# Kernel tuning notes

Measured on AMD Instinct MI355X. Metric: run time of the kernel, lower is better.

## Reference

```python
import jax, jax.numpy as jnp
import numpy as np

N_POINTS = 8192
N_DIM = 2
N_PAIRS = 262144


def setup_inputs() -> dict:
    key = jax.random.key(0)
    k1, k2, k3, k4 = jax.random.split(key, 4)
    logits = jax.random.normal(k1, (N_POINTS, N_DIM), dtype=jnp.float32)
    i = jax.random.randint(k2, (N_PAIRS,), 0, N_POINTS, dtype=jnp.int64)
    j = jax.random.randint(k3, (N_PAIRS,), 0, N_POINTS, dtype=jnp.int64)
    pij = jax.random.uniform(k4, (N_PAIRS,), dtype=jnp.float32, minval=1e-6, maxval=1.0)
    pij = pij / jnp.sum(pij)  # joint probabilities, strictly positive
    return {"pij": pij, "i": i, "j": j, "logits": logits}


def reference(pij, i, j, logits):
    # Pairwise squared distances via the norm expansion (same math as the
    # N x N x D expanded-subtract in the torch original, without the huge tensor).
    sq = jnp.sum(logits * logits, axis=1)                      # [N]
    dkl2 = sq[:, None] + sq[None, :] - 2.0 * (logits @ logits.T)  # [N, N]
    n_diag = logits.shape[0]
    # Student-t partition function, excluding the diagonal (each diag term is 1).
    part = jnp.sum(1.0 / (1.0 + dkl2)) - n_diag
    xi = logits[i]                                              # [E, D]
    xj = logits[j]                                              # [E, D]
    # NOTE: torch adds 1.0 elementwise BEFORE summing over D, so this is
    # (D + ||xi-xj||^2)^-1 — reproduced faithfully.
    num = 1.0 / jnp.sum(1.0 + (xi - xj) ** 2, axis=1)           # [E]
    qij = num / part
    return jnp.sum(pij * (jnp.log(pij) - jnp.log(qij)))
```

## Files before the change

kernel.cpp:

```cpp
#include <hip/hip_runtime.h>
#include <math.h>

#define N_POINTS 8192
#define N_PAIRS  262144

constexpr int BLOCKS  = 1024;
constexpr int THREADS = 256;
constexpr int TILE    = 4;
constexpr int NTILES  = N_POINTS / TILE;
constexpr int EPB     = N_PAIRS / BLOCKS;

typedef float f32x2 __attribute__((ext_vector_type(2)));

__global__ __launch_bounds__(THREADS)
void fused_kernel(const float* __restrict__ logits,
                  const float* __restrict__ pij,
                  const int* __restrict__ ei,
                  const int* __restrict__ ej,
                  float* __restrict__ partials) {
    __shared__ float wred[3][THREADS / 64];

    const int t = threadIdx.x;
    const int b = blockIdx.x;

    const int   ia = ei[b * EPB + t];
    const int   ja = ej[b * EPB + t];
    const float pp = pij[b * EPB + t];

    const float2* __restrict__ pts = (const float2*)logits;

    const int v1 = b;
    const int v2 = NTILES - 1 - b;

    auto sweep = [&](int v) -> float {
        const int r0 = v * TILE;
        f32x2 rxv[TILE], ryv[TILE], acc[TILE];
        #pragma unroll
        for (int r = 0; r < TILE; ++r) {
            const float2 pr = pts[r0 + r];
            rxv[r] = (f32x2){pr.x, pr.x};
            ryv[r] = (f32x2){pr.y, pr.y};
            acc[r] = (f32x2){0.0f, 0.0f};
        }
        #pragma unroll 4
        for (int k = r0 + 2 * t; k < N_POINTS; k += 2 * THREADS) {
            const float4 qq = *(const float4*)&pts[k];
            const f32x2 qx = (f32x2){qq.x, qq.z};
            const f32x2 qy = (f32x2){qq.y, qq.w};
            #pragma unroll
            for (int r = 0; r < TILE; ++r) {
                const f32x2 dx = rxv[r] - qx;
                const f32x2 dy = ryv[r] - qy;
                const f32x2 d2 = dx * dx + dy * dy + 1.0f;
                acc[r] += (f32x2){__builtin_amdgcn_rcpf(d2.x),
                                  __builtin_amdgcn_rcpf(d2.y)};
            }
        }
        float s = 0.0f;
        #pragma unroll
        for (int r = 0; r < TILE; ++r) s += acc[r].x + acc[r].y;
        return s;
    };

    float T = sweep(v1) + sweep(v2);

    float Dc = 0.0f;
    if (t < 2 * TILE * TILE) {
        const int v = (t < TILE * TILE) ? v1 : v2;
        const int l = t & (TILE * TILE - 1);
        const int i = v * TILE + (l >> 2);
        const int k = v * TILE + (l & 3);
        const float dx = pts[i].x - pts[k].x;
        const float dy = pts[i].y - pts[k].y;
        const float d2 = __builtin_fmaf(dx, dx, __builtin_fmaf(dy, dy, 1.0f));
        Dc = __builtin_amdgcn_rcpf(d2);
    }
    float part = __builtin_fmaf(2.0f, T, -Dc);

    float s1, sp;
    {
        const float2 pa = pts[ia], pb = pts[ja];
        const float dx = pa.x - pb.x, dy = pa.y - pb.y;
        const float d2 = __builtin_fmaf(dx, dx, __builtin_fmaf(dy, dy, 2.0f));
        s1 = pp * (__logf(pp) + __logf(d2));
        sp = pp;
    }

    #pragma unroll
    for (int off = 32; off > 0; off >>= 1) {
        part += __shfl_down(part, off, 64);
        s1   += __shfl_down(s1,   off, 64);
        sp   += __shfl_down(sp,   off, 64);
    }
    const int w = t >> 6, l = t & 63;
    if (l == 0) { wred[0][w] = part; wred[1][w] = s1; wred[2][w] = sp; }
    __syncthreads();
    if (t == 0) {
        float r0s = 0.f, r1s = 0.f, r2s = 0.f;
        #pragma unroll
        for (int i = 0; i < THREADS / 64; ++i) {
            r0s += wred[0][i]; r1s += wred[1][i]; r2s += wred[2][i];
        }
        partials[0 * BLOCKS + b] = r0s;
        partials[1 * BLOCKS + b] = r1s;
        partials[2 * BLOCKS + b] = r2s;
    }
}

__global__ __launch_bounds__(256)
void final_kernel(const float* __restrict__ partials, float* __restrict__ out) {
    __shared__ double ra[4], rs[4], rp[4];
    const int t = threadIdx.x;

    double a = 0.0, s = 0.0, p = 0.0;
    #pragma unroll
    for (int q = 0; q < BLOCKS / 256; ++q) {
        a += (double)partials[0 * BLOCKS + t + 256 * q];
        s += (double)partials[1 * BLOCKS + t + 256 * q];
        p += (double)partials[2 * BLOCKS + t + 256 * q];
    }

    #pragma unroll
    for (int off = 32; off > 0; off >>= 1) {
        a += __shfl_down(a, off, 64);
        s += __shfl_down(s, off, 64);
        p += __shfl_down(p, off, 64);
    }
    const int w = t >> 6, l = t & 63;
    if (l == 0) { ra[w] = a; rs[w] = s; rp[w] = p; }
    __syncthreads();
    if (t == 0) {
        double A = 0.0, S = 0.0, P = 0.0;
        #pragma unroll
        for (int i = 0; i < 4; ++i) { A += ra[i]; S += rs[i]; P += rp[i]; }
        A -= (double)N_POINTS;
        out[0] = (float)(S + log(A) * P);
    }
}

extern "C" void kernel_launch(void* const* d_in, const int* in_sizes, int n_in,
                              void* d_out, int out_size, void* d_ws, size_t ws_size,
                              hipStream_t stream) {
    const float* pij    = (const float*)d_in[0];
    const int*   ei     = (const int*)d_in[1];
    const int*   ej     = (const int*)d_in[2];
    const float* logits = (const float*)d_in[3];
    float* out = (float*)d_out;

    float* partials = (float*)d_ws;

    fused_kernel<<<BLOCKS, THREADS, 0, stream>>>(logits, pij, ei, ej, partials);
    final_kernel<<<1, 256, 0, stream>>>(partials, out);
}
```

Measured before the change: 71.48 us.

## Replace symmetric triangular sweep with full square sweep of 8-row tiles

Drops the symmetry-exploiting two-tile triangular sweep and diagonal correction, and instead has each block compute 8 rows against all points with a fixed, fully unrolled loop. This removes the loop-bound variability and the correction step, and it doubles row reuse of each loaded column pair. In exchange the total number of pairwise reciprocal evaluations roughly doubles.

```diff
diff --git a/kernel.cpp b/kernel.cpp
--- a/kernel.cpp
+++ b/kernel.cpp
@@ -6,9 +6,9 @@
 
 constexpr int BLOCKS  = 1024;
 constexpr int THREADS = 256;
-constexpr int TILE    = 4;
-constexpr int NTILES  = N_POINTS / TILE;
+constexpr int TILE    = 8;
 constexpr int EPB     = N_PAIRS / BLOCKS;
+constexpr int KITERS  = N_POINTS / (2 * THREADS);
 
 typedef float f32x2 __attribute__((ext_vector_type(2)));
 
@@ -28,54 +28,35 @@
     const float pp = pij[b * EPB + t];
 
     const float2* __restrict__ pts = (const float2*)logits;
+    const int r0 = b * TILE;
 
-    const int v1 = b;
-    const int v2 = NTILES - 1 - b;
+    f32x2 rxv[TILE], ryv[TILE], acc[TILE];
+    #pragma unroll
+    for (int r = 0; r < TILE; ++r) {
+        const float2 pr = pts[r0 + r];
+        rxv[r] = (f32x2){pr.x, pr.x};
+        ryv[r] = (f32x2){pr.y, pr.y};
+        acc[r] = (f32x2){0.0f, 0.0f};
+    }
 
-    auto sweep = [&](int v) -> float {
-        const int r0 = v * TILE;
-        f32x2 rxv[TILE], ryv[TILE], acc[TILE];
+    #pragma unroll
+    for (int it = 0; it < KITERS; ++it) {
+        const int k = 2 * t + it * (2 * THREADS);
+        const float4 qq = *(const float4*)&pts[k];
+        const f32x2 qx = (f32x2){qq.x, qq.z};
+        const f32x2 qy = (f32x2){qq.y, qq.w};
         #pragma unroll
         for (int r = 0; r < TILE; ++r) {
-            const float2 pr = pts[r0 + r];
-            rxv[r] = (f32x2){pr.x, pr.x};
-            ryv[r] = (f32x2){pr.y, pr.y};
-            acc[r] = (f32x2){0.0f, 0.0f};
+            const f32x2 dx = rxv[r] - qx;
+            const f32x2 dy = ryv[r] - qy;
+            const f32x2 d2 = dx * dx + dy * dy + 1.0f;
+            acc[r] += (f32x2){__builtin_amdgcn_rcpf(d2.x),
+                              __builtin_amdgcn_rcpf(d2.y)};
         }
-        #pragma unroll 4
-        for (int k = r0 + 2 * t; k < N_POINTS; k += 2 * THREADS) {
-            const float4 qq = *(const float4*)&pts[k];
-            const f32x2 qx = (f32x2){qq.x, qq.z};
-            const f32x2 qy = (f32x2){qq.y, qq.w};
-            #pragma unroll
-            for (int r = 0; r < TILE; ++r) {
-                const f32x2 dx = rxv[r] - qx;
-                const f32x2 dy = ryv[r] - qy;
-                const f32x2 d2 = dx * dx + dy * dy + 1.0f;
-                acc[r] += (f32x2){__builtin_amdgcn_rcpf(d2.x),
-                                  __builtin_amdgcn_rcpf(d2.y)};
-            }
-        }
-        float s = 0.0f;
-        #pragma unroll
-        for (int r = 0; r < TILE; ++r) s += acc[r].x + acc[r].y;
-        return s;
-    };
-
-    float T = sweep(v1) + sweep(v2);
-
-    float Dc = 0.0f;
-    if (t < 2 * TILE * TILE) {
-        const int v = (t < TILE * TILE) ? v1 : v2;
-        const int l = t & (TILE * TILE - 1);
-        const int i = v * TILE + (l >> 2);
-        const int k = v * TILE + (l & 3);
-        const float dx = pts[i].x - pts[k].x;
-        const float dy = pts[i].y - pts[k].y;
-        const float d2 = __builtin_fmaf(dx, dx, __builtin_fmaf(dy, dy, 1.0f));
-        Dc = __builtin_amdgcn_rcpf(d2);
     }
-    float part = __builtin_fmaf(2.0f, T, -Dc);
+    float part = 0.0f;
+    #pragma unroll
+    for (int r = 0; r < TILE; ++r) part += acc[r].x + acc[r].y;
 
     float s1, sp;
     {
```

Result: no change. 72.62 us (+1.6%).
